# Kernel optimization log

Hardware: AMD Instinct MI355X
Metric: run time of the kernel (lower is better)

The kernel has to match this reference:

```python
import jax, jax.numpy as jnp
import numpy as np

B, E, H, V, KV = 64, 256, 512, 50257, 2048


def setup_inputs() -> dict:
    key = jax.random.key(0)
    ks = jax.random.split(key, 16)
    s_e = 1.0 / np.sqrt(E)
    s_h = 1.0 / np.sqrt(H)
    s_eh = 1.0 / np.sqrt(E + H)
    return {
        "input": jax.random.randint(ks[0], (B,), 0, V),
        "h0": jax.random.normal(ks[1], (B, H), jnp.float32),
        "c0": jax.random.normal(ks[2], (B, H), jnp.float32),
        "k": jax.random.normal(ks[3], (KV, E), jnp.float32),
        "context_vector": jax.random.normal(ks[4], (B, H), jnp.float32),
        # embedding table
        "embedding": jax.random.normal(ks[5], (V, E), jnp.float32) * 0.02,
        # LSTMCell params (PyTorch layout: gates ordered i,f,g,o)
        "W_ih": jax.random.uniform(ks[6], (4 * H, E), jnp.float32, -s_h, s_h),
        "b_ih": jax.random.uniform(ks[7], (4 * H,), jnp.float32, -s_h, s_h),
        "W_hh": jax.random.uniform(ks[8], (4 * H, H), jnp.float32, -s_h, s_h),
        "b_hh": jax.random.uniform(ks[9], (4 * H,), jnp.float32, -s_h, s_h),
        # attn_key MLP: Linear(E+H,E) -> tanh -> Linear(E,E) -> tanh -> Linear(E,1)
        "W1": jax.random.uniform(ks[10], (E, E + H), jnp.float32, -s_eh, s_eh),
        "b1": jnp.zeros((E,), jnp.float32),
        "W2": jax.random.uniform(ks[11], (E, E), jnp.float32, -s_e, s_e),
        "b2": jnp.zeros((E,), jnp.float32),
        "W3": jax.random.uniform(ks[12], (1, E), jnp.float32, -s_e, s_e),
        "b3": jnp.zeros((1,), jnp.float32),
        # output projection Linear(H, V)
        "W_out": jax.random.uniform(ks[13], (V, H), jnp.float32, -s_h, s_h),
        "b_out": jax.random.uniform(ks[14], (V,), jnp.float32, -s_h, s_h),
    }


def reference(input, h0, c0, k, context_vector, embedding, W_ih, b_ih, W_hh, b_hh,
              W1, b1, W2, b2, W3, b3, W_out, b_out):
    # embedding lookup (dropout in eval mode = identity)
    x = embedding[input]  # (B, E)
    # LSTMCell
    gates = x @ W_ih.T + b_ih + h0 @ W_hh.T + b_hh  # (B, 4H)
    i, f, g, o = jnp.split(gates, 4, axis=-1)
    i = jax.nn.sigmoid(i)
    f = jax.nn.sigmoid(f)
    g = jnp.tanh(g)
    o = jax.nn.sigmoid(o)
    c_t = f * c0 + i * g
    h_t = o * jnp.tanh(c_t)  # (B, H)
    # key attention: broadcast h_t over kv keys, keys over batch (torch.cat-repeat in original)
    h_b = jnp.broadcast_to(h_t[:, None, :], (B, KV, H))
    k_b = jnp.broadcast_to(k[None, :, :], (B, KV, E))
    feat = jnp.concatenate([h_b, k_b], axis=-1)  # (B, KV, H+E)
    u = jnp.tanh(feat @ W1.T + b1)
    u = jnp.tanh(u @ W2.T + b2)
    scores = (u @ W3.T + b3)[..., 0]  # (B, KV)
    # vocab logits; original pads V-KV zeros in front then adds -> scores hit last KV slots
    o_t = h_t @ W_out.T + b_out  # (B, V)
    o_t = o_t.at[:, V - KV:].add(scores)
    y_t = jax.nn.log_softmax(o_t, axis=-1)
    return (y_t, h_t, c_t)
```

## Files before the change

### kernel.cpp

```cpp
#include <hip/hip_runtime.h>
#include <math.h>

namespace {

constexpr int B = 64, E = 256, H = 512, V = 50257, KV = 2048;
constexpr int NOUT = (V + 63) / 64;
constexpr int PSTRIDE = 800;

typedef __bf16 bf16x8 __attribute__((ext_vector_type(8)));
typedef float f32x4 __attribute__((ext_vector_type(4)));

__device__ __forceinline__ float fast_tanh(float x) {
  float e = __expf(2.f * x);
  return 1.f - 2.f / (e + 1.f);
}
__device__ __forceinline__ float sigmoidf(float x) {
  return 1.f / (1.f + __expf(-x));
}
__device__ __forceinline__ f32x4 mfma16(bf16x8 a, bf16x8 b, f32x4 c) {
  return __builtin_amdgcn_mfma_f32_16x16x32_bf16(a, b, c, 0, 0, 0);
}

__global__ __launch_bounds__(256) void k_gates(const int* __restrict__ inp,
    const float* __restrict__ h0, const float* __restrict__ emb,
    const float* __restrict__ W_ih, const float* __restrict__ b_ih,
    const float* __restrict__ W_hh, const float* __restrict__ b_hh,
    float* __restrict__ gates) {
  int b = threadIdx.x & 63;
  int j = blockIdx.x * 4 + (threadIdx.x >> 6);
  j = __builtin_amdgcn_readfirstlane(j);
  int row = inp[b];
  const float* xr = emb + (long)row * E;
  const float* wi = W_ih + (long)j * E;
  const float* hr = h0 + b * H;
  const float* wh = W_hh + (long)j * H;
  float acc = b_ih[j] + b_hh[j];
#pragma unroll 8
  for (int t = 0; t < E / 4; ++t) {
    float4 x4 = ((const float4*)xr)[t];
    float4 w4 = ((const float4*)wi)[t];
    acc += x4.x * w4.x + x4.y * w4.y + x4.z * w4.z + x4.w * w4.w;
  }
#pragma unroll 8
  for (int t = 0; t < H / 4; ++t) {
    float4 h4 = ((const float4*)hr)[t];
    float4 w4 = ((const float4*)wh)[t];
    acc += h4.x * w4.x + h4.y * w4.y + h4.z * w4.z + h4.w * w4.w;
  }
  gates[j * B + b] = acc;
}

__global__ __launch_bounds__(256) void k_lstm(const float* __restrict__ gates,
    const float* __restrict__ c0, float* __restrict__ out_h, float* __restrict__ out_c,
    __bf16* __restrict__ hp) {
  int i = blockIdx.x * 256 + threadIdx.x;
  int b = i >> 9, hh = i & 511;
  float gi = gates[(hh)*B + b];
  float gf = gates[(hh + 512) * B + b];
  float gg = gates[(hh + 1024) * B + b];
  float go = gates[(hh + 1536) * B + b];
  float c = sigmoidf(gf) * c0[i] + sigmoidf(gi) * fast_tanh(gg);
  float h = sigmoidf(go) * fast_tanh(c);
  out_h[i] = h;
  out_c[i] = c;
  hp[((hh >> 3) * 64 + b) * 8 + (hh & 7)] = (__bf16)h;
}

__global__ __launch_bounds__(256) void k_prep(const float* __restrict__ h_t,
    const float* __restrict__ W1, const float* __restrict__ b1,
    const float* __restrict__ k, const float* __restrict__ W2,
    float* __restrict__ Ah, float* __restrict__ Kp, __bf16* __restrict__ W2p) {
  __shared__ float ks_[64][257];
  int bid = blockIdx.x;
  int t = threadIdx.x;
  if (bid < 64) {
    int b = t & 63;
    int e = bid * 4 + (t >> 6);
    e = __builtin_amdgcn_readfirstlane(e);
    const float* hr = h_t + b * H;
    const float* wr = W1 + (long)e * (E + H);
    float acc = b1[e];
#pragma unroll 8
    for (int q = 0; q < H / 4; ++q) {
      float4 h4 = ((const float4*)hr)[q];
      float4 w4 = ((const float4*)wr)[q];
      acc += h4.x * w4.x + h4.y * w4.y + h4.z * w4.z + h4.w * w4.w;
    }
    Ah[b * E + e] = acc;
  } else if (bid < 192) {
    int t2 = bid - 64;
    int kv0 = (t2 & 31) * 64;
    int e0 = (t2 >> 5) * 64;
    for (int i = 0; i < 16; ++i) {
      int idx = i * 256 + t;
      int rr = idx >> 6, cc = (idx & 63) * 4;
      float4 v = *(const float4*)(k + (kv0 + rr) * E + cc);
      ks_[rr][cc] = v.x; ks_[rr][cc + 1] = v.y; ks_[rr][cc + 2] = v.z; ks_[rr][cc + 3] = v.w;
    }
    __syncthreads();
    int r0 = (t >> 4);
    int c0 = (t & 15) * 4;
    float acc[4][4] = {};
    const float* w0 = W1 + (long)(e0 + c0) * (E + H) + H;
    for (int kk = 0; kk < 256; kk += 4) {
      float4 w[4];
#pragma unroll
      for (int c = 0; c < 4; ++c) w[c] = *(const float4*)(w0 + (long)c * (E + H) + kk);
#pragma unroll
      for (int q = 0; q < 4; ++q) {
#pragma unroll
        for (int r = 0; r < 4; ++r) {
          float kvv = ks_[r0 + 16 * r][kk + q];
#pragma unroll
          for (int c = 0; c < 4; ++c) acc[r][c] += kvv * ((const float*)&w[c])[q];
        }
      }
    }
    for (int r = 0; r < 4; ++r)
      for (int c = 0; c < 4; ++c)
        Kp[(kv0 + r0 + 16 * r) * E + e0 + c0 + c] = acc[r][c];
  } else {
    int idx = (bid - 192) * 256 + t;
    int kk = idx >> 8, n = idx & 255;
    W2p[((kk >> 3) * 256 + n) * 8 + (kk & 7)] = (__bf16)W2[n * 256 + kk];
  }
}

__global__ __launch_bounds__(256) void k_attn(const float* __restrict__ Ah,
    const float* __restrict__ Kp, const __bf16* __restrict__ W2p,
    const float* __restrict__ b2, const float* __restrict__ W3, const float* __restrict__ b3,
    float* __restrict__ scoresT) {
  __shared__ __align__(16) unsigned char lds_[64 * 256 * 2];
  int tid = threadIdx.x;
  int blk = blockIdx.x;
  int b = blk >> 5;
  int kv0 = (blk & 31) * 64;
  for (int i = 0; i < 8; ++i) {
    int idx = i * 256 + tid;
    int row = idx >> 5;
    int k0 = (idx & 31) * 8;
    const float* ap = Ah + b * E + k0;
    const float* kp = Kp + (kv0 + row) * E + k0;
    float4 a0 = *(const float4*)ap;
    float4 a1 = *(const float4*)(ap + 4);
    float4 p0 = *(const float4*)kp;
    float4 p1 = *(const float4*)(kp + 4);
    bf16x8 u;
    u[0] = (__bf16)fast_tanh(a0.x + p0.x);
    u[1] = (__bf16)fast_tanh(a0.y + p0.y);
    u[2] = (__bf16)fast_tanh(a0.z + p0.z);
    u[3] = (__bf16)fast_tanh(a0.w + p0.w);
    u[4] = (__bf16)fast_tanh(a1.x + p1.x);
    u[5] = (__bf16)fast_tanh(a1.y + p1.y);
    u[6] = (__bf16)fast_tanh(a1.z + p1.z);
    u[7] = (__bf16)fast_tanh(a1.w + p1.w);
    int byte = (row * 512 + k0 * 2) ^ ((row & 7) << 4);
    *(bf16x8*)(lds_ + byte) = u;
  }
  __syncthreads();
  int l = tid & 63, wc = tid >> 6;
  int lr = l & 15, lg = l >> 4;
  float b2v[4], w3v[4];
#pragma unroll
  for (int nf = 0; nf < 4; ++nf) {
    int col = wc * 64 + nf * 16 + lr;
    b2v[nf] = b2[col];
    w3v[nf] = W3[col];
  }
  f32x4 acc[4][4] = {};
  for (int ks = 0; ks < 8; ++ks) {
    bf16x8 a[4], bf[4];
#pragma unroll
    for (int mf = 0; mf < 4; ++mf) {
      int row = mf * 16 + lr;
      int byte = (row * 512 + (ks * 32 + lg * 8) * 2) ^ ((row & 7) << 4);
      a[mf] = *(const bf16x8*)(lds_ + byte);
    }
#pragma unroll
    for (int nf = 0; nf < 4; ++nf) {
      int col = wc * 64 + nf * 16 + lr;
      bf[nf] = *(const bf16x8*)(W2p + ((ks * 4 + lg) * 256 + col) * 8);
    }
#pragma unroll
    for (int mf = 0; mf < 4; ++mf)
#pragma unroll
      for (int nf = 0; nf < 4; ++nf)
        acc[mf][nf] = mfma16(a[mf], bf[nf], acc[mf][nf]);
  }
  float p[4][4];
#pragma unroll
  for (int mf = 0; mf < 4; ++mf)
#pragma unroll
    for (int r = 0; r < 4; ++r) p[mf][r] = 0.f;
#pragma unroll
  for (int mf = 0; mf < 4; ++mf)
#pragma unroll
    for (int nf = 0; nf < 4; ++nf)
#pragma unroll
      for (int r = 0; r < 4; ++r) {
        float u2 = fast_tanh(acc[mf][nf][r] + b2v[nf]);
        p[mf][r] += u2 * w3v[nf];
      }
#pragma unroll
  for (int off = 1; off < 16; off <<= 1)
#pragma unroll
    for (int mf = 0; mf < 4; ++mf)
#pragma unroll
      for (int r = 0; r < 4; ++r) p[mf][r] += __shfl_xor(p[mf][r], off);
  __syncthreads();
  float* red = (float*)lds_;
  if (lr == 0) {
#pragma unroll
    for (int mf = 0; mf < 4; ++mf)
#pragma unroll
      for (int r = 0; r < 4; ++r) red[(mf * 16 + lg * 4 + r) * 4 + wc] = p[mf][r];
  }
  __syncthreads();
  if (tid < 64) {
    float s = red[tid * 4 + 0] + red[tid * 4 + 1] + red[tid * 4 + 2] + red[tid * 4 + 3] + b3[0];
    scoresT[(kv0 + tid) * 64 + b] = s;
  }
}

__global__ __launch_bounds__(256) void k_out(const __bf16* __restrict__ hp,
    const float* __restrict__ W_out, const float* __restrict__ b_out,
    const float* __restrict__ scoresT, float* __restrict__ o,
    float* __restrict__ pm, float* __restrict__ ps) {
  __shared__ __align__(16) unsigned char lds_[64 * 256 * 2];
  __shared__ float rm[64][4], rs[64][4];
  int tid = threadIdx.x;
  int l = tid & 63, wn = tid >> 6;
  int lr = l & 15, lg = l >> 4;
  int col0 = blockIdx.x * 64;
  f32x4 acc[4] = {};
#pragma unroll
  for (int hh = 0; hh < 2; ++hh) {
    if (hh) __syncthreads();
#pragma unroll
    for (int i = 0; i < 8; ++i) {
      int u = i * 256 + tid;
      int row = u >> 5;
      int c16 = u & 31;
      int rr = col0 + row; if (rr > V - 1) rr = V - 1;
      const float* p = W_out + (long)rr * H + hh * 256 + c16 * 8;
      float4 w0 = *(const float4*)p;
      float4 w1 = *(const float4*)(p + 4);
      bf16x8 v;
      v[0] = (__bf16)w0.x; v[1] = (__bf16)w0.y; v[2] = (__bf16)w0.z; v[3] = (__bf16)w0.w;
      v[4] = (__bf16)w1.x; v[5] = (__bf16)w1.y; v[6] = (__bf16)w1.z; v[7] = (__bf16)w1.w;
      int byte = (row * 512 + c16 * 16) ^ ((row & 7) << 4);
      *(bf16x8*)(lds_ + byte) = v;
    }
    __syncthreads();
    int r = wn * 16 + lr;
    int rbase = r * 512;
    int rsw = (r & 7) << 4;
#pragma unroll
    for (int ks2 = 0; ks2 < 8; ++ks2) {
      int ksg = hh * 8 + ks2;
      bf16x8 a[4];
#pragma unroll
      for (int mf = 0; mf < 4; ++mf)
        a[mf] = *(const bf16x8*)(hp + ((ksg * 4 + lg) * 64 + mf * 16 + lr) * 8);
      bf16x8 bv = *(const bf16x8*)(lds_ + ((rbase + ks2 * 64 + lg * 16) ^ rsw));
#pragma unroll
      for (int mf = 0; mf < 4; ++mf) acc[mf] = mfma16(a[mf], bv, acc[mf]);
    }
  }
  __syncthreads();
  float (*vbuf)[65] = (float(*)[65])lds_;
  int col = col0 + wn * 16 + lr;
  bool valid = col < V;
  float bo = valid ? b_out[col] : 0.f;
  bool has = valid && col >= (V - KV);
  int scix = col - (V - KV);
#pragma unroll
  for (int mf = 0; mf < 4; ++mf)
#pragma unroll
    for (int r = 0; r < 4; ++r) {
      int m = mf * 16 + lg * 4 + r;
      float v = acc[mf][r] + bo;
      if (has) v += scoresT[scix * 64 + m];
      if (!valid) v = -1e30f;
      vbuf[m][wn * 16 + lr] = v;
    }
  __syncthreads();
  int nvalid = V - col0; if (nvalid > 64) nvalid = 64;
#pragma unroll
  for (int i = 0; i < 16; ++i) {
    int idx = i * 256 + tid;
    int m = idx >> 6, c = idx & 63;
    if (c < nvalid) o[(long)m * V + col0 + c] = vbuf[m][c];
  }
  int row = tid & 63, g = tid >> 6;
  float mm = -1e30f;
#pragma unroll
  for (int c = 0; c < 16; ++c) mm = fmaxf(mm, vbuf[row][g * 16 + c]);
  float ssum = 0.f;
#pragma unroll
  for (int c = 0; c < 16; ++c) ssum += __expf(vbuf[row][g * 16 + c] - mm);
  rm[row][g] = mm; rs[row][g] = ssum;
  __syncthreads();
  if (tid < 64) {
    float M = fmaxf(fmaxf(rm[tid][0], rm[tid][1]), fmaxf(rm[tid][2], rm[tid][3]));
    float S = 0.f;
#pragma unroll
    for (int g2 = 0; g2 < 4; ++g2) S += rs[tid][g2] * __expf(rm[tid][g2] - M);
    pm[tid * PSTRIDE + blockIdx.x] = M;
    ps[tid * PSTRIDE + blockIdx.x] = S;
  }
}

__global__ __launch_bounds__(256) void k_z(const float* __restrict__ pm,
    const float* __restrict__ ps, float* __restrict__ logZ) {
  int r = blockIdx.x;
  int tid = threadIdx.x;
  float m = -1e30f, s = 0.f;
  for (int p = tid; p < NOUT; p += 256) {
    float om = pm[r * PSTRIDE + p];
    float os = ps[r * PSTRIDE + p];
    float M = fmaxf(m, om);
    s = s * __expf(m - M) + os * __expf(om - M);
    m = M;
  }
#pragma unroll
  for (int off = 1; off < 64; off <<= 1) {
    float om = __shfl_xor(m, off);
    float os = __shfl_xor(s, off);
    float M = fmaxf(m, om);
    s = s * __expf(m - M) + os * __expf(om - M);
    m = M;
  }
  __shared__ float sm[4], ss[4];
  int w = tid >> 6;
  if ((tid & 63) == 0) { sm[w] = m; ss[w] = s; }
  __syncthreads();
  if (tid == 0) {
    m = sm[0]; s = ss[0];
    for (int i = 1; i < 4; ++i) {
      float M = fmaxf(m, sm[i]);
      s = s * __expf(m - M) + ss[i] * __expf(sm[i] - M);
      m = M;
    }
    logZ[r] = m + __logf(s);
  }
}

__global__ __launch_bounds__(256) void k_sub(float* __restrict__ o, const float* __restrict__ logZ) {
  int r = blockIdx.y;
  float z = logZ[r];
  int i0 = (blockIdx.x * 256 + threadIdx.x) * 4;
  float* row = o + (long)r * V;
  if (i0 + 3 < V) {
    float4 v = *(float4*)(row + i0);
    v.x -= z; v.y -= z; v.z -= z; v.w -= z;
    *(float4*)(row + i0) = v;
  } else {
    for (int i = i0; i < V; ++i) row[i] -= z;
  }
}

}

extern "C" void kernel_launch(void* const* d_in, const int* in_sizes, int n_in,
                              void* d_out, int out_size, void* d_ws, size_t ws_size,
                              hipStream_t stream) {
  const int* inp = (const int*)d_in[0];
  const float* h0 = (const float*)d_in[1];
  const float* c0 = (const float*)d_in[2];
  const float* kk = (const float*)d_in[3];
  const float* emb = (const float*)d_in[5];
  const float* W_ih = (const float*)d_in[6];
  const float* b_ih = (const float*)d_in[7];
  const float* W_hh = (const float*)d_in[8];
  const float* b_hh = (const float*)d_in[9];
  const float* W1 = (const float*)d_in[10];
  const float* b1 = (const float*)d_in[11];
  const float* W2 = (const float*)d_in[12];
  const float* b2 = (const float*)d_in[13];
  const float* W3 = (const float*)d_in[14];
  const float* b3 = (const float*)d_in[15];
  const float* W_out = (const float*)d_in[16];
  const float* b_out = (const float*)d_in[17];

  float* y = (float*)d_out;
  float* h_t = y + (size_t)B * V;
  float* c_t = h_t + (size_t)B * H;

  char* ws = (char*)d_ws;
  float* gates = (float*)ws;                 ws += (size_t)4 * H * B * 4;
  float* Ah = (float*)ws;                    ws += (size_t)B * E * 4;
  float* Kp = (float*)ws;                    ws += (size_t)KV * E * 4;
  float* scoresT = (float*)ws;               ws += (size_t)B * KV * 4;
  float* logZ = (float*)ws;                  ws += 256;
  float* pm = (float*)ws;                    ws += (size_t)B * PSTRIDE * 4;
  float* ps = (float*)ws;                    ws += (size_t)B * PSTRIDE * 4;
  __bf16* W2p = (__bf16*)ws;                 ws += (size_t)E * E * 2;
  __bf16* hp = (__bf16*)ws;                  ws += (size_t)B * H * 2;

  hipLaunchKernelGGL(k_gates, dim3(4 * H / 4), dim3(256), 0, stream,
                     inp, h0, emb, W_ih, b_ih, W_hh, b_hh, gates);
  hipLaunchKernelGGL(k_lstm, dim3(B * H / 256), dim3(256), 0, stream, gates, c0, h_t, c_t, hp);
  hipLaunchKernelGGL(k_prep, dim3(448), dim3(256), 0, stream,
                     h_t, W1, b1, kk, W2, Ah, Kp, W2p);
  hipLaunchKernelGGL(k_attn, dim3(B * KV / 64), dim3(256), 0, stream,
                     Ah, Kp, W2p, b2, W3, b3, scoresT);
  hipLaunchKernelGGL(k_out, dim3(NOUT), dim3(256), 0, stream,
                     hp, W_out, b_out, scoresT, y, pm, ps);
  hipLaunchKernelGGL(k_z, dim3(B), dim3(256), 0, stream, pm, ps, logZ);
  hipLaunchKernelGGL(k_sub, dim3((V + 1023) / 1024, B), dim3(256), 0, stream, y, logZ);
}
```

Before: 166.7 us.

## Split k_out K dimension across two wave groups with 512-thread blocks

```diff
diff --git a/kernel.cpp b/kernel.cpp
--- a/kernel.cpp
+++ b/kernel.cpp
@@ -222,90 +222,114 @@
   }
 }
 
-__global__ __launch_bounds__(256) void k_out(const __bf16* __restrict__ hp,
+__global__ __launch_bounds__(512) void k_out(const __bf16* __restrict__ hp,
     const float* __restrict__ W_out, const float* __restrict__ b_out,
     const float* __restrict__ scoresT, float* __restrict__ o,
     float* __restrict__ pm, float* __restrict__ ps) {
-  __shared__ __align__(16) unsigned char lds_[64 * 256 * 2];
-  __shared__ float rm[64][4], rs[64][4];
+  __shared__ __align__(16) unsigned char lds_[64 * 512 * 2];
+  __shared__ float rm[64][8], rs[64][8];
   int tid = threadIdx.x;
-  int l = tid & 63, wn = tid >> 6;
-  int lr = l & 15, lg = l >> 4;
+  int wave = tid >> 6;
+  int kh = wave >> 2;
+  int wn = wave & 3;
+  int l = tid & 63;
+  int lr = l & 15, lg = (l >> 4) & 3;
   int col0 = blockIdx.x * 64;
+#pragma unroll
+  for (int i = 0; i < 8; ++i) {
+    int u = i * 512 + tid;
+    int row = u >> 6;
+    int c16 = u & 63;
+    int rr = col0 + row; if (rr > V - 1) rr = V - 1;
+    const float* p = W_out + (long)rr * H + c16 * 8;
+    float4 w0 = *(const float4*)p;
+    float4 w1 = *(const float4*)(p + 4);
+    bf16x8 v;
+    v[0] = (__bf16)w0.x; v[1] = (__bf16)w0.y; v[2] = (__bf16)w0.z; v[3] = (__bf16)w0.w;
+    v[4] = (__bf16)w1.x; v[5] = (__bf16)w1.y; v[6] = (__bf16)w1.z; v[7] = (__bf16)w1.w;
+    int byte = (row * 1024 + c16 * 16) ^ ((row & 7) << 4);
+    *(bf16x8*)(lds_ + byte) = v;
+  }
+  __syncthreads();
+  int r = wn * 16 + lr;
+  int rbase = r * 1024;
+  int rsw = (r & 7) << 4;
   f32x4 acc[4] = {};
-#pragma unroll
-  for (int hh = 0; hh < 2; ++hh) {
-    if (hh) __syncthreads();
-#pragma unroll
-    for (int i = 0; i < 8; ++i) {
-      int u = i * 256 + tid;
-      int row = u >> 5;
-      int c16 = u & 31;
-      int rr = col0 + row; if (rr > V - 1) rr = V - 1;
-      const float* p = W_out + (long)rr * H + hh * 256 + c16 * 8;
-      float4 w0 = *(const float4*)p;
-      float4 w1 = *(const float4*)(p + 4);
-      bf16x8 v;
-      v[0] = (__bf16)w0.x; v[1] = (__bf16)w0.y; v[2] = (__bf16)w0.z; v[3] = (__bf16)w0.w;
-      v[4] = (__bf16)w1.x; v[5] = (__bf16)w1.y; v[6] = (__bf16)w1.z; v[7] = (__bf16)w1.w;
-      int byte = (row * 512 + c16 * 16) ^ ((row & 7) << 4);
-      *(bf16x8*)(lds_ + byte) = v;
-    }
-    __syncthreads();
-    int r = wn * 16 + lr;
-    int rbase = r * 512;
-    int rsw = (r & 7) << 4;
-#pragma unroll
-    for (int ks2 = 0; ks2 < 8; ++ks2) {
-      int ksg = hh * 8 + ks2;
-      bf16x8 a[4];
+  bf16x8 a_n[4], b_n;
+  {
+    int ksg = kh * 8;
+#pragma unroll
+    for (int mf = 0; mf < 4; ++mf)
+      a_n[mf] = *(const bf16x8*)(hp + ((ksg * 4 + lg) * 64 + mf * 16 + lr) * 8);
+    b_n = *(const bf16x8*)(lds_ + ((rbase + ksg * 64 + lg * 16) ^ rsw));
+  }
+#pragma unroll
+  for (int ks2 = 0; ks2 < 8; ++ks2) {
+    bf16x8 a_c[4]; bf16x8 b_c = b_n;
+#pragma unroll
+    for (int mf = 0; mf < 4; ++mf) a_c[mf] = a_n[mf];
+    if (ks2 < 7) {
+      int ksg = kh * 8 + ks2 + 1;
 #pragma unroll
       for (int mf = 0; mf < 4; ++mf)
-        a[mf] = *(const bf16x8*)(hp + ((ksg * 4 + lg) * 64 + mf * 16 + lr) * 8);
-      bf16x8 bv = *(const bf16x8*)(lds_ + ((rbase + ks2 * 64 + lg * 16) ^ rsw));
-#pragma unroll
-      for (int mf = 0; mf < 4; ++mf) acc[mf] = mfma16(a[mf], bv, acc[mf]);
-    }
-  }
-  __syncthreads();
-  float (*vbuf)[65] = (float(*)[65])lds_;
-  int col = col0 + wn * 16 + lr;
-  bool valid = col < V;
-  float bo = valid ? b_out[col] : 0.f;
-  bool has = valid && col >= (V - KV);
-  int scix = col - (V - KV);
-#pragma unroll
-  for (int mf = 0; mf < 4; ++mf)
-#pragma unroll
-    for (int r = 0; r < 4; ++r) {
-      int m = mf * 16 + lg * 4 + r;
-      float v = acc[mf][r] + bo;
-      if (has) v += scoresT[scix * 64 + m];
-      if (!valid) v = -1e30f;
-      vbuf[m][wn * 16 + lr] = v;
-    }
+        a_n[mf] = *(const bf16x8*)(hp + ((ksg * 4 + lg) * 64 + mf * 16 + lr) * 8);
+      b_n = *(const bf16x8*)(lds_ + ((rbase + ksg * 64 + lg * 16) ^ rsw));
+    }
+#pragma unroll
+    for (int mf = 0; mf < 4; ++mf) acc[mf] = mfma16(a_c[mf], b_c, acc[mf]);
+  }
+  __syncthreads();
+  float* red = (float*)lds_;
+  if (kh == 1) {
+#pragma unroll
+    for (int mf = 0; mf < 4; ++mf)
+#pragma unroll
+      for (int rr2 = 0; rr2 < 4; ++rr2)
+        red[(mf * 16 + lg * 4 + rr2) * 64 + wn * 16 + lr] = acc[mf][rr2];
+  }
+  __syncthreads();
+  float (*vbuf)[65] = (float(*)[65])(lds_ + 16384);
+  if (kh == 0) {
+    int col = col0 + wn * 16 + lr;
+    bool valid = col < V;
+    float bo = valid ? b_out[col] : 0.f;
+    bool has = valid && col >= (V - KV);
+    int scix = col - (V - KV);
+#pragma unroll
+    for (int mf = 0; mf < 4; ++mf)
+#pragma unroll
+      for (int rr2 = 0; rr2 < 4; ++rr2) {
+        int m = mf * 16 + lg * 4 + rr2;
+        float v = acc[mf][rr2] + red[m * 64 + wn * 16 + lr] + bo;
+        if (has) v += scoresT[scix * 64 + m];
+        if (!valid) v = -1e30f;
+        vbuf[m][wn * 16 + lr] = v;
+      }
+  }
   __syncthreads();
   int nvalid = V - col0; if (nvalid > 64) nvalid = 64;
 #pragma unroll
-  for (int i = 0; i < 16; ++i) {
-    int idx = i * 256 + tid;
+  for (int i = 0; i < 8; ++i) {
+    int idx = i * 512 + tid;
     int m = idx >> 6, c = idx & 63;
     if (c < nvalid) o[(long)m * V + col0 + c] = vbuf[m][c];
   }
   int row = tid & 63, g = tid >> 6;
   float mm = -1e30f;
 #pragma unroll
-  for (int c = 0; c < 16; ++c) mm = fmaxf(mm, vbuf[row][g * 16 + c]);
+  for (int c = 0; c < 8; ++c) mm = fmaxf(mm, vbuf[row][g * 8 + c]);
   float ssum = 0.f;
 #pragma unroll
-  for (int c = 0; c < 16; ++c) ssum += __expf(vbuf[row][g * 16 + c] - mm);
+  for (int c = 0; c < 8; ++c) ssum += __expf(vbuf[row][g * 8 + c] - mm);
   rm[row][g] = mm; rs[row][g] = ssum;
   __syncthreads();
   if (tid < 64) {
-    float M = fmaxf(fmaxf(rm[tid][0], rm[tid][1]), fmaxf(rm[tid][2], rm[tid][3]));
+    float M = rm[tid][0];
+#pragma unroll
+    for (int g2 = 1; g2 < 8; ++g2) M = fmaxf(M, rm[tid][g2]);
     float S = 0.f;
 #pragma unroll
-    for (int g2 = 0; g2 < 4; ++g2) S += rs[tid][g2] * __expf(rm[tid][g2] - M);
+    for (int g2 = 0; g2 < 8; ++g2) S += rs[tid][g2] * __expf(rm[tid][g2] - M);
     pm[tid * PSTRIDE + blockIdx.x] = M;
     ps[tid * PSTRIDE + blockIdx.x] = S;
   }
@@ -405,7 +429,7 @@
                      h_t, W1, b1, kk, W2, Ah, Kp, W2p);
   hipLaunchKernelGGL(k_attn, dim3(B * KV / 64), dim3(256), 0, stream,
                      Ah, Kp, W2p, b2, W3, b3, scoresT);
-  hipLaunchKernelGGL(k_out, dim3(NOUT), dim3(256), 0, stream,
+  hipLaunchKernelGGL(k_out, dim3(NOUT), dim3(512), 0, stream,
                      hp, W_out, b_out, scoresT, y, pm, ps);
   hipLaunchKernelGGL(k_z, dim3(B), dim3(256), 0, stream, pm, ps, logZ);
   hipLaunchKernelGGL(k_sub, dim3((V + 1023) / 1024, B), dim3(256), 0, stream, y, logZ);
```

After: 170.2 us. 2.1% more time.

## Pre-pack W_out into bf16 k-major layout in a separate kernel

Applied to the files above, without the earlier changes.

```diff
diff --git a/kernel.cpp b/kernel.cpp
--- a/kernel.cpp
+++ b/kernel.cpp
@@ -5,6 +5,7 @@
 
 constexpr int B = 64, E = 256, H = 512, V = 50257, KV = 2048;
 constexpr int NOUT = (V + 63) / 64;
+constexpr int VP = NOUT * 64;
 constexpr int PSTRIDE = 800;
 
 typedef __bf16 bf16x8 __attribute__((ext_vector_type(8)));
@@ -19,6 +20,36 @@
 }
 __device__ __forceinline__ f32x4 mfma16(bf16x8 a, bf16x8 b, f32x4 c) {
   return __builtin_amdgcn_mfma_f32_16x16x32_bf16(a, b, c, 0, 0, 0);
+}
+
+__global__ __launch_bounds__(256) void k_packw(const float* __restrict__ W_out,
+                                               __bf16* __restrict__ Wp) {
+  __shared__ __align__(16) unsigned char lds_[64 * 512 * 2];
+  int tid = threadIdx.x;
+  int col0 = blockIdx.x * 64;
+#pragma unroll
+  for (int i = 0; i < 16; ++i) {
+    int u = i * 256 + tid;
+    int row = u >> 6, k8 = u & 63;
+    int rr = col0 + row; if (rr > V - 1) rr = V - 1;
+    const float* p = W_out + (long)rr * H + k8 * 8;
+    float4 w0 = *(const float4*)p;
+    float4 w1 = *(const float4*)(p + 4);
+    bf16x8 v;
+    v[0] = (__bf16)w0.x; v[1] = (__bf16)w0.y; v[2] = (__bf16)w0.z; v[3] = (__bf16)w0.w;
+    v[4] = (__bf16)w1.x; v[5] = (__bf16)w1.y; v[6] = (__bf16)w1.z; v[7] = (__bf16)w1.w;
+    int byte = (row * 1024 + k8 * 16) ^ ((row & 7) << 4);
+    *(bf16x8*)(lds_ + byte) = v;
+  }
+  __syncthreads();
+#pragma unroll
+  for (int i = 0; i < 16; ++i) {
+    int u = i * 256 + tid;
+    int k8 = u >> 6, colt = u & 63;
+    int byte = (colt * 1024 + k8 * 16) ^ ((colt & 7) << 4);
+    bf16x8 v = *(const bf16x8*)(lds_ + byte);
+    *(bf16x8*)(Wp + ((long)k8 * VP + col0 + colt) * 8) = v;
+  }
 }
 
 __global__ __launch_bounds__(256) void k_gates(const int* __restrict__ inp,
@@ -223,53 +254,27 @@
 }
 
 __global__ __launch_bounds__(256) void k_out(const __bf16* __restrict__ hp,
-    const float* __restrict__ W_out, const float* __restrict__ b_out,
+    const __bf16* __restrict__ Wp, const float* __restrict__ b_out,
     const float* __restrict__ scoresT, float* __restrict__ o,
     float* __restrict__ pm, float* __restrict__ ps) {
-  __shared__ __align__(16) unsigned char lds_[64 * 256 * 2];
+  __shared__ float vbuf[64][65];
   __shared__ float rm[64][4], rs[64][4];
   int tid = threadIdx.x;
   int l = tid & 63, wn = tid >> 6;
   int lr = l & 15, lg = l >> 4;
   int col0 = blockIdx.x * 64;
+  int col = col0 + wn * 16 + lr;
   f32x4 acc[4] = {};
 #pragma unroll
-  for (int hh = 0; hh < 2; ++hh) {
-    if (hh) __syncthreads();
-#pragma unroll
-    for (int i = 0; i < 8; ++i) {
-      int u = i * 256 + tid;
-      int row = u >> 5;
-      int c16 = u & 31;
-      int rr = col0 + row; if (rr > V - 1) rr = V - 1;
-      const float* p = W_out + (long)rr * H + hh * 256 + c16 * 8;
-      float4 w0 = *(const float4*)p;
-      float4 w1 = *(const float4*)(p + 4);
-      bf16x8 v;
-      v[0] = (__bf16)w0.x; v[1] = (__bf16)w0.y; v[2] = (__bf16)w0.z; v[3] = (__bf16)w0.w;
-      v[4] = (__bf16)w1.x; v[5] = (__bf16)w1.y; v[6] = (__bf16)w1.z; v[7] = (__bf16)w1.w;
-      int byte = (row * 512 + c16 * 16) ^ ((row & 7) << 4);
-      *(bf16x8*)(lds_ + byte) = v;
-    }
-    __syncthreads();
-    int r = wn * 16 + lr;
-    int rbase = r * 512;
-    int rsw = (r & 7) << 4;
-#pragma unroll
-    for (int ks2 = 0; ks2 < 8; ++ks2) {
-      int ksg = hh * 8 + ks2;
-      bf16x8 a[4];
-#pragma unroll
-      for (int mf = 0; mf < 4; ++mf)
-        a[mf] = *(const bf16x8*)(hp + ((ksg * 4 + lg) * 64 + mf * 16 + lr) * 8);
-      bf16x8 bv = *(const bf16x8*)(lds_ + ((rbase + ks2 * 64 + lg * 16) ^ rsw));
-#pragma unroll
-      for (int mf = 0; mf < 4; ++mf) acc[mf] = mfma16(a[mf], bv, acc[mf]);
-    }
-  }
-  __syncthreads();
-  float (*vbuf)[65] = (float(*)[65])lds_;
-  int col = col0 + wn * 16 + lr;
+  for (int ks = 0; ks < 16; ++ks) {
+    bf16x8 a[4];
+#pragma unroll
+    for (int mf = 0; mf < 4; ++mf)
+      a[mf] = *(const bf16x8*)(hp + ((ks * 4 + lg) * 64 + mf * 16 + lr) * 8);
+    bf16x8 bv = *(const bf16x8*)(Wp + ((long)(ks * 4 + lg) * VP + col) * 8);
+#pragma unroll
+    for (int mf = 0; mf < 4; ++mf) acc[mf] = mfma16(a[mf], bv, acc[mf]);
+  }
   bool valid = col < V;
   float bo = valid ? b_out[col] : 0.f;
   bool has = valid && col >= (V - KV);
@@ -397,7 +402,10 @@
   float* ps = (float*)ws;                    ws += (size_t)B * PSTRIDE * 4;
   __bf16* W2p = (__bf16*)ws;                 ws += (size_t)E * E * 2;
   __bf16* hp = (__bf16*)ws;                  ws += (size_t)B * H * 2;
-
+  ws = (char*)(((size_t)ws + 255) & ~(size_t)255);
+  __bf16* Wp = (__bf16*)ws;                  ws += (size_t)VP * H * 2;
+
+  hipLaunchKernelGGL(k_packw, dim3(NOUT), dim3(256), 0, stream, W_out, Wp);
   hipLaunchKernelGGL(k_gates, dim3(4 * H / 4), dim3(256), 0, stream,
                      inp, h0, emb, W_ih, b_ih, W_hh, b_hh, gates);
   hipLaunchKernelGGL(k_lstm, dim3(B * H / 256), dim3(256), 0, stream, gates, c0, h_t, c_t, hp);
@@ -406,7 +414,7 @@
   hipLaunchKernelGGL(k_attn, dim3(B * KV / 64), dim3(256), 0, stream,
                      Ah, Kp, W2p, b2, W3, b3, scoresT);
   hipLaunchKernelGGL(k_out, dim3(NOUT), dim3(256), 0, stream,
-                     hp, W_out, b_out, scoresT, y, pm, ps);
+                     hp, Wp, b_out, scoresT, y, pm, ps);
   hipLaunchKernelGGL(k_z, dim3(B), dim3(256), 0, stream, pm, ps, logZ);
   hipLaunchKernelGGL(k_sub, dim3((V + 1023) / 1024, B), dim3(256), 0, stream, y, logZ);
 }
```

Result: slower. 182.9 us (+9.7%).

## Merge all stages into one cooperative persistent kernel with grid syncs

Applied to the files above, without the earlier changes.

```diff
diff --git a/kernel.cpp b/kernel.cpp
--- a/kernel.cpp
+++ b/kernel.cpp
@@ -1,5 +1,8 @@
 #include <hip/hip_runtime.h>
+#include <hip/hip_cooperative_groups.h>
 #include <math.h>
+
+namespace cg = cooperative_groups;
 
 namespace {
 
@@ -21,63 +24,109 @@
   return __builtin_amdgcn_mfma_f32_16x16x32_bf16(a, b, c, 0, 0, 0);
 }
 
-__global__ __launch_bounds__(256) void k_gates(const int* __restrict__ inp,
-    const float* __restrict__ h0, const float* __restrict__ emb,
+__global__ __launch_bounds__(256, 3) void mono(
+    const int* __restrict__ inp, const float* __restrict__ h0,
+    const float* __restrict__ c0, const float* __restrict__ kkey,
+    const float* __restrict__ emb,
     const float* __restrict__ W_ih, const float* __restrict__ b_ih,
     const float* __restrict__ W_hh, const float* __restrict__ b_hh,
-    float* __restrict__ gates) {
-  int b = threadIdx.x & 63;
-  int j = blockIdx.x * 4 + (threadIdx.x >> 6);
-  j = __builtin_amdgcn_readfirstlane(j);
-  int row = inp[b];
-  const float* xr = emb + (long)row * E;
-  const float* wi = W_ih + (long)j * E;
-  const float* hr = h0 + b * H;
-  const float* wh = W_hh + (long)j * H;
-  float acc = b_ih[j] + b_hh[j];
+    const float* __restrict__ W1, const float* __restrict__ b1,
+    const float* __restrict__ W2, const float* __restrict__ b2,
+    const float* __restrict__ W3, const float* __restrict__ b3,
+    const float* __restrict__ W_out, const float* __restrict__ b_out,
+    float* __restrict__ y, float* __restrict__ h_t, float* __restrict__ c_t,
+    float* __restrict__ Ah, float* __restrict__ Kp, float* __restrict__ scoresT,
+    float* __restrict__ logZ, float* __restrict__ pm, float* __restrict__ ps,
+    __bf16* __restrict__ W2p, __bf16* __restrict__ hp) {
+  __shared__ __align__(16) unsigned char SM[32896];
+  __shared__ float g4[4][64];
+  __shared__ float rm[64][4], rs[64][4];
+  __shared__ float sm2[4], ss2[4];
+  cg::grid_group grid = cg::this_grid();
+  int tid = threadIdx.x, bid = blockIdx.x, nb = gridDim.x;
+
+  for (int t = bid; t < 1024; t += nb) {
+    if (t < 512) {
+      int hh = t;
+      int jq = tid >> 6, b = tid & 63;
+      int j = jq * 512 + hh;
+      int row = inp[b];
+      const float* xr = emb + (long)row * E;
+      const float* wi = W_ih + (long)j * E;
+      const float* hr = h0 + (long)b * H;
+      const float* wh = W_hh + (long)j * H;
+      float acc = b_ih[j] + b_hh[j];
 #pragma unroll 8
-  for (int t = 0; t < E / 4; ++t) {
-    float4 x4 = ((const float4*)xr)[t];
-    float4 w4 = ((const float4*)wi)[t];
-    acc += x4.x * w4.x + x4.y * w4.y + x4.z * w4.z + x4.w * w4.w;
-  }
+      for (int q = 0; q < E / 4; ++q) {
+        float4 x4 = ((const float4*)xr)[q];
+        float4 w4 = ((const float4*)wi)[q];
+        acc += x4.x * w4.x + x4.y * w4.y + x4.z * w4.z + x4.w * w4.w;
+      }
 #pragma unroll 8
-  for (int t = 0; t < H / 4; ++t) {
-    float4 h4 = ((const float4*)hr)[t];
-    float4 w4 = ((const float4*)wh)[t];
-    acc += h4.x * w4.x + h4.y * w4.y + h4.z * w4.z + h4.w * w4.w;
-  }
-  gates[j * B + b] = acc;
-}
-
-__global__ __launch_bounds__(256) void k_lstm(const float* __restrict__ gates,
-    const float* __restrict__ c0, float* __restrict__ out_h, float* __restrict__ out_c,
-    __bf16* __restrict__ hp) {
-  int i = blockIdx.x * 256 + threadIdx.x;
-  int b = i >> 9, hh = i & 511;
-  float gi = gates[(hh)*B + b];
-  float gf = gates[(hh + 512) * B + b];
-  float gg = gates[(hh + 1024) * B + b];
-  float go = gates[(hh + 1536) * B + b];
-  float c = sigmoidf(gf) * c0[i] + sigmoidf(gi) * fast_tanh(gg);
-  float h = sigmoidf(go) * fast_tanh(c);
-  out_h[i] = h;
-  out_c[i] = c;
-  hp[((hh >> 3) * 64 + b) * 8 + (hh & 7)] = (__bf16)h;
-}
-
-__global__ __launch_bounds__(256) void k_prep(const float* __restrict__ h_t,
-    const float* __restrict__ W1, const float* __restrict__ b1,
-    const float* __restrict__ k, const float* __restrict__ W2,
-    float* __restrict__ Ah, float* __restrict__ Kp, __bf16* __restrict__ W2p) {
-  __shared__ float ks_[64][257];
-  int bid = blockIdx.x;
-  int t = threadIdx.x;
+      for (int q = 0; q < H / 4; ++q) {
+        float4 h4 = ((const float4*)hr)[q];
+        float4 w4 = ((const float4*)wh)[q];
+        acc += h4.x * w4.x + h4.y * w4.y + h4.z * w4.z + h4.w * w4.w;
+      }
+      g4[jq][b] = acc;
+      __syncthreads();
+      if (tid < 64) {
+        int bb = tid;
+        float cc = sigmoidf(g4[1][bb]) * c0[bb * H + hh] +
+                   sigmoidf(g4[0][bb]) * fast_tanh(g4[2][bb]);
+        float hv = sigmoidf(g4[3][bb]) * fast_tanh(cc);
+        h_t[bb * H + hh] = hv;
+        c_t[bb * H + hh] = cc;
+        hp[((hh >> 3) * 64 + bb) * 8 + (hh & 7)] = (__bf16)hv;
+      }
+    } else if (t < 768) {
+      float(*ks2)[257] = (float(*)[257])SM;
+      int kt = t - 512;
+      int kv0 = (kt & 63) * 32;
+      int e0 = (kt >> 6) * 64;
+#pragma unroll
+      for (int i = 0; i < 8; ++i) {
+        int idx = i * 256 + tid;
+        int rr = idx >> 6, ccc = (idx & 63) * 4;
+        float4 v = *(const float4*)(kkey + (long)(kv0 + rr) * E + ccc);
+        ks2[rr][ccc] = v.x; ks2[rr][ccc + 1] = v.y;
+        ks2[rr][ccc + 2] = v.z; ks2[rr][ccc + 3] = v.w;
+      }
+      __syncthreads();
+      int r0 = tid >> 4;
+      int c0e = (tid & 15) * 4;
+      float acc[2][4] = {};
+      const float* w0 = W1 + (long)(e0 + c0e) * (E + H) + H;
+      for (int kk = 0; kk < 256; kk += 4) {
+        float4 w[4];
+#pragma unroll
+        for (int c = 0; c < 4; ++c) w[c] = *(const float4*)(w0 + (long)c * (E + H) + kk);
+#pragma unroll
+        for (int q = 0; q < 4; ++q) {
+#pragma unroll
+          for (int r = 0; r < 2; ++r) {
+            float kvv = ks2[r0 + 16 * r][kk + q];
+#pragma unroll
+            for (int c = 0; c < 4; ++c) acc[r][c] += kvv * ((const float*)&w[c])[q];
+          }
+        }
+      }
+      for (int r = 0; r < 2; ++r)
+        for (int c = 0; c < 4; ++c)
+          Kp[(long)(kv0 + r0 + 16 * r) * E + e0 + c0e + c] = acc[r][c];
+    } else {
+      int idx = (t - 768) * 256 + tid;
+      int kk = idx >> 8, n = idx & 255;
+      W2p[((kk >> 3) * 256 + n) * 8 + (kk & 7)] = (__bf16)W2[n * 256 + kk];
+    }
+    __syncthreads();
+  }
+  grid.sync();
+
   if (bid < 64) {
-    int b = t & 63;
-    int e = bid * 4 + (t >> 6);
-    e = __builtin_amdgcn_readfirstlane(e);
-    const float* hr = h_t + b * H;
+    int b = tid & 63;
+    int e = bid * 4 + (tid >> 6);
+    const float* hr = h_t + (long)b * H;
     const float* wr = W1 + (long)e * (E + H);
     float acc = b1[e];
 #pragma unroll 8
@@ -87,276 +136,234 @@
       acc += h4.x * w4.x + h4.y * w4.y + h4.z * w4.z + h4.w * w4.w;
     }
     Ah[b * E + e] = acc;
-  } else if (bid < 192) {
-    int t2 = bid - 64;
-    int kv0 = (t2 & 31) * 64;
-    int e0 = (t2 >> 5) * 64;
-    for (int i = 0; i < 16; ++i) {
-      int idx = i * 256 + t;
-      int rr = idx >> 6, cc = (idx & 63) * 4;
-      float4 v = *(const float4*)(k + (kv0 + rr) * E + cc);
-      ks_[rr][cc] = v.x; ks_[rr][cc + 1] = v.y; ks_[rr][cc + 2] = v.z; ks_[rr][cc + 3] = v.w;
-    }
-    __syncthreads();
-    int r0 = (t >> 4);
-    int c0 = (t & 15) * 4;
-    float acc[4][4] = {};
-    const float* w0 = W1 + (long)(e0 + c0) * (E + H) + H;
-    for (int kk = 0; kk < 256; kk += 4) {
-      float4 w[4];
-#pragma unroll
-      for (int c = 0; c < 4; ++c) w[c] = *(const float4*)(w0 + (long)c * (E + H) + kk);
-#pragma unroll
-      for (int q = 0; q < 4; ++q) {
-#pragma unroll
-        for (int r = 0; r < 4; ++r) {
-          float kvv = ks_[r0 + 16 * r][kk + q];
-#pragma unroll
-          for (int c = 0; c < 4; ++c) acc[r][c] += kvv * ((const float*)&w[c])[q];
-        }
-      }
-    }
-    for (int r = 0; r < 4; ++r)
-      for (int c = 0; c < 4; ++c)
-        Kp[(kv0 + r0 + 16 * r) * E + e0 + c0 + c] = acc[r][c];
-  } else {
-    int idx = (bid - 192) * 256 + t;
-    int kk = idx >> 8, n = idx & 255;
-    W2p[((kk >> 3) * 256 + n) * 8 + (kk & 7)] = (__bf16)W2[n * 256 + kk];
-  }
-}
-
-__global__ __launch_bounds__(256) void k_attn(const float* __restrict__ Ah,
-    const float* __restrict__ Kp, const __bf16* __restrict__ W2p,
-    const float* __restrict__ b2, const float* __restrict__ W3, const float* __restrict__ b3,
-    float* __restrict__ scoresT) {
-  __shared__ __align__(16) unsigned char lds_[64 * 256 * 2];
-  int tid = threadIdx.x;
-  int blk = blockIdx.x;
-  int b = blk >> 5;
-  int kv0 = (blk & 31) * 64;
-  for (int i = 0; i < 8; ++i) {
-    int idx = i * 256 + tid;
-    int row = idx >> 5;
-    int k0 = (idx & 31) * 8;
-    const float* ap = Ah + b * E + k0;
-    const float* kp = Kp + (kv0 + row) * E + k0;
-    float4 a0 = *(const float4*)ap;
-    float4 a1 = *(const float4*)(ap + 4);
-    float4 p0 = *(const float4*)kp;
-    float4 p1 = *(const float4*)(kp + 4);
-    bf16x8 u;
-    u[0] = (__bf16)fast_tanh(a0.x + p0.x);
-    u[1] = (__bf16)fast_tanh(a0.y + p0.y);
-    u[2] = (__bf16)fast_tanh(a0.z + p0.z);
-    u[3] = (__bf16)fast_tanh(a0.w + p0.w);
-    u[4] = (__bf16)fast_tanh(a1.x + p1.x);
-    u[5] = (__bf16)fast_tanh(a1.y + p1.y);
-    u[6] = (__bf16)fast_tanh(a1.z + p1.z);
-    u[7] = (__bf16)fast_tanh(a1.w + p1.w);
-    int byte = (row * 512 + k0 * 2) ^ ((row & 7) << 4);
-    *(bf16x8*)(lds_ + byte) = u;
-  }
-  __syncthreads();
-  int l = tid & 63, wc = tid >> 6;
-  int lr = l & 15, lg = l >> 4;
-  float b2v[4], w3v[4];
-#pragma unroll
-  for (int nf = 0; nf < 4; ++nf) {
-    int col = wc * 64 + nf * 16 + lr;
-    b2v[nf] = b2[col];
-    w3v[nf] = W3[col];
-  }
-  f32x4 acc[4][4] = {};
-  for (int ks = 0; ks < 8; ++ks) {
-    bf16x8 a[4], bf[4];
-#pragma unroll
-    for (int mf = 0; mf < 4; ++mf) {
-      int row = mf * 16 + lr;
-      int byte = (row * 512 + (ks * 32 + lg * 8) * 2) ^ ((row & 7) << 4);
-      a[mf] = *(const bf16x8*)(lds_ + byte);
-    }
+  }
+  grid.sync();
+
+  for (int t = bid; t < 2048; t += nb) {
+    int b = t >> 5;
+    int kv0 = (t & 31) * 64;
+    for (int i = 0; i < 8; ++i) {
+      int idx = i * 256 + tid;
+      int row = idx >> 5;
+      int k0 = (idx & 31) * 8;
+      const float* ap = Ah + b * E + k0;
+      const float* kp = Kp + (long)(kv0 + row) * E + k0;
+      float4 a0 = *(const float4*)ap;
+      float4 a1 = *(const float4*)(ap + 4);
+      float4 p0 = *(const float4*)kp;
+      float4 p1 = *(const float4*)(kp + 4);
+      bf16x8 u;
+      u[0] = (__bf16)fast_tanh(a0.x + p0.x);
+      u[1] = (__bf16)fast_tanh(a0.y + p0.y);
+      u[2] = (__bf16)fast_tanh(a0.z + p0.z);
+      u[3] = (__bf16)fast_tanh(a0.w + p0.w);
+      u[4] = (__bf16)fast_tanh(a1.x + p1.x);
+      u[5] = (__bf16)fast_tanh(a1.y + p1.y);
+      u[6] = (__bf16)fast_tanh(a1.z + p1.z);
+      u[7] = (__bf16)fast_tanh(a1.w + p1.w);
+      int byte = (row * 512 + k0 * 2) ^ ((row & 7) << 4);
+      *(bf16x8*)(SM + byte) = u;
+    }
+    __syncthreads();
+    int l = tid & 63, wc = tid >> 6;
+    int lr = l & 15, lg = l >> 4;
+    float b2v[4], w3v[4];
 #pragma unroll
     for (int nf = 0; nf < 4; ++nf) {
       int col = wc * 64 + nf * 16 + lr;
-      bf[nf] = *(const bf16x8*)(W2p + ((ks * 4 + lg) * 256 + col) * 8);
-    }
+      b2v[nf] = b2[col];
+      w3v[nf] = W3[col];
+    }
+    f32x4 acc[4][4] = {};
+    for (int ks = 0; ks < 8; ++ks) {
+      bf16x8 a[4], bf[4];
+#pragma unroll
+      for (int mf = 0; mf < 4; ++mf) {
+        int row = mf * 16 + lr;
+        int byte = (row * 512 + (ks * 32 + lg * 8) * 2) ^ ((row & 7) << 4);
+        a[mf] = *(const bf16x8*)(SM + byte);
+      }
+#pragma unroll
+      for (int nf = 0; nf < 4; ++nf) {
+        int col = wc * 64 + nf * 16 + lr;
+        bf[nf] = *(const bf16x8*)(W2p + ((ks * 4 + lg) * 256 + col) * 8);
+      }
+#pragma unroll
+      for (int mf = 0; mf < 4; ++mf)
+#pragma unroll
+        for (int nf = 0; nf < 4; ++nf)
+          acc[mf][nf] = mfma16(a[mf], bf[nf], acc[mf][nf]);
+    }
+    float p[4][4];
 #pragma unroll
     for (int mf = 0; mf < 4; ++mf)
 #pragma unroll
+      for (int r = 0; r < 4; ++r) p[mf][r] = 0.f;
+#pragma unroll
+    for (int mf = 0; mf < 4; ++mf)
+#pragma unroll
       for (int nf = 0; nf < 4; ++nf)
-        acc[mf][nf] = mfma16(a[mf], bf[nf], acc[mf][nf]);
-  }
-  float p[4][4];
-#pragma unroll
-  for (int mf = 0; mf < 4; ++mf)
-#pragma unroll
-    for (int r = 0; r < 4; ++r) p[mf][r] = 0.f;
-#pragma unroll
-  for (int mf = 0; mf < 4; ++mf)
-#pragma unroll
-    for (int nf = 0; nf < 4; ++nf)
+#pragma unroll
+        for (int r = 0; r < 4; ++r) {
+          float u2 = fast_tanh(acc[mf][nf][r] + b2v[nf]);
+          p[mf][r] += u2 * w3v[nf];
+        }
+#pragma unroll
+    for (int off = 1; off < 16; off <<= 1)
+#pragma unroll
+      for (int mf = 0; mf < 4; ++mf)
+#pragma unroll
+        for (int r = 0; r < 4; ++r) p[mf][r] += __shfl_xor(p[mf][r], off);
+    __syncthreads();
+    float* red = (float*)SM;
+    if (lr == 0) {
+#pragma unroll
+      for (int mf = 0; mf < 4; ++mf)
+#pragma unroll
+        for (int r = 0; r < 4; ++r) red[(mf * 16 + lg * 4 + r) * 4 + wc] = p[mf][r];
+    }
+    __syncthreads();
+    if (tid < 64) {
+      float s = red[tid * 4 + 0] + red[tid * 4 + 1] + red[tid * 4 + 2] + red[tid * 4 + 3] + b3[0];
+      scoresT[(long)(kv0 + tid) * 64 + b] = s;
+    }
+    __syncthreads();
+  }
+  grid.sync();
+
+  for (int t = bid; t < NOUT; t += nb) {
+    int l = tid & 63, wn = tid >> 6;
+    int lr = l & 15, lg = l >> 4;
+    int col0 = t * 64;
+    f32x4 acc[4] = {};
+#pragma unroll
+    for (int hhf = 0; hhf < 2; ++hhf) {
+      if (hhf) __syncthreads();
+#pragma unroll
+      for (int i = 0; i < 8; ++i) {
+        int u = i * 256 + tid;
+        int row = u >> 5;
+        int c16 = u & 31;
+        int rr = col0 + row; if (rr > V - 1) rr = V - 1;
+        const float* p = W_out + (long)rr * H + hhf * 256 + c16 * 8;
+        float4 w0 = *(const float4*)p;
+        float4 w1 = *(const float4*)(p + 4);
+        bf16x8 v;
+        v[0] = (__bf16)w0.x; v[1] = (__bf16)w0.y; v[2] = (__bf16)w0.z; v[3] = (__bf16)w0.w;
+        v[4] = (__bf16)w1.x; v[5] = (__bf16)w1.y; v[6] = (__bf16)w1.z; v[7] = (__bf16)w1.w;
+        int byte = (row * 512 + c16 * 16) ^ ((row & 7) << 4);
+        *(bf16x8*)(SM + byte) = v;
+      }
+      __syncthreads();
+      int r = wn * 16 + lr;
+      int rbase = r * 512;
+      int rsw = (r & 7) << 4;
+#pragma unroll
+      for (int ks2 = 0; ks2 < 8; ++ks2) {
+        int ksg = hhf * 8 + ks2;
+        bf16x8 a[4];
+#pragma unroll
+        for (int mf = 0; mf < 4; ++mf)
+          a[mf] = *(const bf16x8*)(hp + ((ksg * 4 + lg) * 64 + mf * 16 + lr) * 8);
+        bf16x8 bv = *(const bf16x8*)(SM + ((rbase + ks2 * 64 + lg * 16) ^ rsw));
+#pragma unroll
+        for (int mf = 0; mf < 4; ++mf) acc[mf] = mfma16(a[mf], bv, acc[mf]);
+      }
+    }
+    __syncthreads();
+    float(*vbuf)[65] = (float(*)[65])SM;
+    int col = col0 + wn * 16 + lr;
+    bool valid = col < V;
+    float bo = valid ? b_out[col] : 0.f;
+    bool has = valid && col >= (V - KV);
+    int scix = col - (V - KV);
+#pragma unroll
+    for (int mf = 0; mf < 4; ++mf)
 #pragma unroll
       for (int r = 0; r < 4; ++r) {
-        float u2 = fast_tanh(acc[mf][nf][r] + b2v[nf]);
-        p[mf][r] += u2 * w3v[nf];
-      }
-#pragma unroll
-  for (int off = 1; off < 16; off <<= 1)
-#pragma unroll
-    for (int mf = 0; mf < 4; ++mf)
-#pragma unroll
-      for (int r = 0; r < 4; ++r) p[mf][r] += __shfl_xor(p[mf][r], off);
-  __syncthreads();
-  float* red = (float*)lds_;
-  if (lr == 0) {
-#pragma unroll
-    for (int mf = 0; mf < 4; ++mf)
-#pragma unroll
-      for (int r = 0; r < 4; ++r) red[(mf * 16 + lg * 4 + r) * 4 + wc] = p[mf][r];
-  }
-  __syncthreads();
-  if (tid < 64) {
-    float s = red[tid * 4 + 0] + red[tid * 4 + 1] + red[tid * 4 + 2] + red[tid * 4 + 3] + b3[0];
-    scoresT[(kv0 + tid) * 64 + b] = s;
-  }
-}
-
-__global__ __launch_bounds__(256) void k_out(const __bf16* __restrict__ hp,
-    const float* __restrict__ W_out, const float* __restrict__ b_out,
-    const float* __restrict__ scoresT, float* __restrict__ o,
-    float* __restrict__ pm, float* __restrict__ ps) {
-  __shared__ __align__(16) unsigned char lds_[64 * 256 * 2];
-  __shared__ float rm[64][4], rs[64][4];
-  int tid = threadIdx.x;
-  int l = tid & 63, wn = tid >> 6;
-  int lr = l & 15, lg = l >> 4;
-  int col0 = blockIdx.x * 64;
-  f32x4 acc[4] = {};
-#pragma unroll
-  for (int hh = 0; hh < 2; ++hh) {
-    if (hh) __syncthreads();
-#pragma unroll
-    for (int i = 0; i < 8; ++i) {
-      int u = i * 256 + tid;
-      int row = u >> 5;
-      int c16 = u & 31;
-      int rr = col0 + row; if (rr > V - 1) rr = V - 1;
-      const float* p = W_out + (long)rr * H + hh * 256 + c16 * 8;
-      float4 w0 = *(const float4*)p;
-      float4 w1 = *(const float4*)(p + 4);
-      bf16x8 v;
-      v[0] = (__bf16)w0.x; v[1] = (__bf16)w0.y; v[2] = (__bf16)w0.z; v[3] = (__bf16)w0.w;
-      v[4] = (__bf16)w1.x; v[5] = (__bf16)w1.y; v[6] = (__bf16)w1.z; v[7] = (__bf16)w1.w;
-      int byte = (row * 512 + c16 * 16) ^ ((row & 7) << 4);
-      *(bf16x8*)(lds_ + byte) = v;
-    }
-    __syncthreads();
-    int r = wn * 16 + lr;
-    int rbase = r * 512;
-    int rsw = (r & 7) << 4;
-#pragma unroll
-    for (int ks2 = 0; ks2 < 8; ++ks2) {
-      int ksg = hh * 8 + ks2;
-      bf16x8 a[4];
-#pragma unroll
-      for (int mf = 0; mf < 4; ++mf)
-        a[mf] = *(const bf16x8*)(hp + ((ksg * 4 + lg) * 64 + mf * 16 + lr) * 8);
-      bf16x8 bv = *(const bf16x8*)(lds_ + ((rbase + ks2 * 64 + lg * 16) ^ rsw));
-#pragma unroll
-      for (int mf = 0; mf < 4; ++mf) acc[mf] = mfma16(a[mf], bv, acc[mf]);
-    }
-  }
-  __syncthreads();
-  float (*vbuf)[65] = (float(*)[65])lds_;
-  int col = col0 + wn * 16 + lr;
-  bool valid = col < V;
-  float bo = valid ? b_out[col] : 0.f;
-  bool has = valid && col >= (V - KV);
-  int scix = col - (V - KV);
-#pragma unroll
-  for (int mf = 0; mf < 4; ++mf)
-#pragma unroll
-    for (int r = 0; r < 4; ++r) {
-      int m = mf * 16 + lg * 4 + r;
-      float v = acc[mf][r] + bo;
-      if (has) v += scoresT[scix * 64 + m];
-      if (!valid) v = -1e30f;
-      vbuf[m][wn * 16 + lr] = v;
-    }
-  __syncthreads();
-  int nvalid = V - col0; if (nvalid > 64) nvalid = 64;
-#pragma unroll
-  for (int i = 0; i < 16; ++i) {
-    int idx = i * 256 + tid;
-    int m = idx >> 6, c = idx & 63;
-    if (c < nvalid) o[(long)m * V + col0 + c] = vbuf[m][c];
-  }
-  int row = tid & 63, g = tid >> 6;
-  float mm = -1e30f;
-#pragma unroll
-  for (int c = 0; c < 16; ++c) mm = fmaxf(mm, vbuf[row][g * 16 + c]);
-  float ssum = 0.f;
-#pragma unroll
-  for (int c = 0; c < 16; ++c) ssum += __expf(vbuf[row][g * 16 + c] - mm);
-  rm[row][g] = mm; rs[row][g] = ssum;
-  __syncthreads();
-  if (tid < 64) {
-    float M = fmaxf(fmaxf(rm[tid][0], rm[tid][1]), fmaxf(rm[tid][2], rm[tid][3]));
-    float S = 0.f;
-#pragma unroll
-    for (int g2 = 0; g2 < 4; ++g2) S += rs[tid][g2] * __expf(rm[tid][g2] - M);
-    pm[tid * PSTRIDE + blockIdx.x] = M;
-    ps[tid * PSTRIDE + blockIdx.x] = S;
-  }
-}
-
-__global__ __launch_bounds__(256) void k_z(const float* __restrict__ pm,
-    const float* __restrict__ ps, float* __restrict__ logZ) {
-  int r = blockIdx.x;
-  int tid = threadIdx.x;
-  float m = -1e30f, s = 0.f;
-  for (int p = tid; p < NOUT; p += 256) {
-    float om = pm[r * PSTRIDE + p];
-    float os = ps[r * PSTRIDE + p];
-    float M = fmaxf(m, om);
-    s = s * __expf(m - M) + os * __expf(om - M);
-    m = M;
-  }
-#pragma unroll
-  for (int off = 1; off < 64; off <<= 1) {
-    float om = __shfl_xor(m, off);
-    float os = __shfl_xor(s, off);
-    float M = fmaxf(m, om);
-    s = s * __expf(m - M) + os * __expf(om - M);
-    m = M;
-  }
-  __shared__ float sm[4], ss[4];
-  int w = tid >> 6;
-  if ((tid & 63) == 0) { sm[w] = m; ss[w] = s; }
-  __syncthreads();
-  if (tid == 0) {
-    m = sm[0]; s = ss[0];
-    for (int i = 1; i < 4; ++i) {
-      float M = fmaxf(m, sm[i]);
-      s = s * __expf(m - M) + ss[i] * __expf(sm[i] - M);
+        int m = mf * 16 + lg * 4 + r;
+        float v = acc[mf][r] + bo;
+        if (has) v += scoresT[(long)scix * 64 + m];
+        if (!valid) v = -1e30f;
+        vbuf[m][wn * 16 + lr] = v;
+      }
+    __syncthreads();
+    int nvalid = V - col0; if (nvalid > 64) nvalid = 64;
+#pragma unroll
+    for (int i = 0; i < 16; ++i) {
+      int idx = i * 256 + tid;
+      int m = idx >> 6, c = idx & 63;
+      if (c < nvalid) y[(long)m * V + col0 + c] = vbuf[m][c];
+    }
+    int row = tid & 63, g = tid >> 6;
+    float mm = -1e30f;
+#pragma unroll
+    for (int c = 0; c < 16; ++c) mm = fmaxf(mm, vbuf[row][g * 16 + c]);
+    float ssum = 0.f;
+#pragma unroll
+    for (int c = 0; c < 16; ++c) ssum += __expf(vbuf[row][g * 16 + c] - mm);
+    rm[row][g] = mm; rs[row][g] = ssum;
+    __syncthreads();
+    if (tid < 64) {
+      float M = fmaxf(fmaxf(rm[tid][0], rm[tid][1]), fmaxf(rm[tid][2], rm[tid][3]));
+      float S = 0.f;
+#pragma unroll
+      for (int g2 = 0; g2 < 4; ++g2) S += rs[tid][g2] * __expf(rm[tid][g2] - M);
+      pm[tid * PSTRIDE + t] = M;
+      ps[tid * PSTRIDE + t] = S;
+    }
+    __syncthreads();
+  }
+  grid.sync();
+
+  if (bid < 64) {
+    int r = bid;
+    float m = -1e30f, s = 0.f;
+    for (int p = tid; p < NOUT; p += 256) {
+      float om = pm[r * PSTRIDE + p];
+      float os = ps[r * PSTRIDE + p];
+      float M = fmaxf(m, om);
+      s = s * __expf(m - M) + os * __expf(om - M);
       m = M;
     }
-    logZ[r] = m + __logf(s);
-  }
-}
-
-__global__ __launch_bounds__(256) void k_sub(float* __restrict__ o, const float* __restrict__ logZ) {
-  int r = blockIdx.y;
-  float z = logZ[r];
-  int i0 = (blockIdx.x * 256 + threadIdx.x) * 4;
-  float* row = o + (long)r * V;
-  if (i0 + 3 < V) {
-    float4 v = *(float4*)(row + i0);
-    v.x -= z; v.y -= z; v.z -= z; v.w -= z;
-    *(float4*)(row + i0) = v;
-  } else {
-    for (int i = i0; i < V; ++i) row[i] -= z;
+#pragma unroll
+    for (int off = 1; off < 64; off <<= 1) {
+      float om = __shfl_xor(m, off);
+      float os = __shfl_xor(s, off);
+      float M = fmaxf(m, om);
+      s = s * __expf(m - M) + os * __expf(om - M);
+      m = M;
+    }
+    int w = tid >> 6;
+    if ((tid & 63) == 0) { sm2[w] = m; ss2[w] = s; }
+    __syncthreads();
+    if (tid == 0) {
+      m = sm2[0]; s = ss2[0];
+      for (int i = 1; i < 4; ++i) {
+        float M = fmaxf(m, sm2[i]);
+        s = s * __expf(m - M) + ss2[i] * __expf(sm2[i] - M);
+        m = M;
+      }
+      logZ[r] = m + __logf(s);
+    }
+  }
+  grid.sync();
+
+  constexpr int SLOTS = (V + 3) / 4;
+  int total4 = 64 * SLOTS;
+  int stride = nb * 256;
+  for (int i4 = bid * 256 + tid; i4 < total4; i4 += stride) {
+    int r = i4 / SLOTS;
+    int c_el = (i4 - r * SLOTS) * 4;
+    float z = logZ[r];
+    float* rowp = y + (long)r * V;
+    if (c_el + 3 < V) {
+      float4 v = *(float4*)(rowp + c_el);
+      v.x -= z; v.y -= z; v.z -= z; v.w -= z;
+      *(float4*)(rowp + c_el) = v;
+    } else {
+      for (int c2 = c_el; c2 < V; ++c2) rowp[c2] -= z;
+    }
   }
 }
 
@@ -368,7 +375,7 @@
   const int* inp = (const int*)d_in[0];
   const float* h0 = (const float*)d_in[1];
   const float* c0 = (const float*)d_in[2];
-  const float* kk = (const float*)d_in[3];
+  const float* kkey = (const float*)d_in[3];
   const float* emb = (const float*)d_in[5];
   const float* W_ih = (const float*)d_in[6];
   const float* b_ih = (const float*)d_in[7];
@@ -388,7 +395,6 @@
   float* c_t = h_t + (size_t)B * H;
 
   char* ws = (char*)d_ws;
-  float* gates = (float*)ws;                 ws += (size_t)4 * H * B * 4;
   float* Ah = (float*)ws;                    ws += (size_t)B * E * 4;
   float* Kp = (float*)ws;                    ws += (size_t)KV * E * 4;
   float* scoresT = (float*)ws;               ws += (size_t)B * KV * 4;
@@ -398,15 +404,21 @@
   __bf16* W2p = (__bf16*)ws;                 ws += (size_t)E * E * 2;
   __bf16* hp = (__bf16*)ws;                  ws += (size_t)B * H * 2;
 
-  hipLaunchKernelGGL(k_gates, dim3(4 * H / 4), dim3(256), 0, stream,
-                     inp, h0, emb, W_ih, b_ih, W_hh, b_hh, gates);
-  hipLaunchKernelGGL(k_lstm, dim3(B * H / 256), dim3(256), 0, stream, gates, c0, h_t, c_t, hp);
-  hipLaunchKernelGGL(k_prep, dim3(448), dim3(256), 0, stream,
-                     h_t, W1, b1, kk, W2, Ah, Kp, W2p);
-  hipLaunchKernelGGL(k_attn, dim3(B * KV / 64), dim3(256), 0, stream,
-                     Ah, Kp, W2p, b2, W3, b3, scoresT);
-  hipLaunchKernelGGL(k_out, dim3(NOUT), dim3(256), 0, stream,
-                     hp, W_out, b_out, scoresT, y, pm, ps);
-  hipLaunchKernelGGL(k_z, dim3(B), dim3(256), 0, stream, pm, ps, logZ);
-  hipLaunchKernelGGL(k_sub, dim3((V + 1023) / 1024, B), dim3(256), 0, stream, y, logZ);
-}
+  int occ = 0;
+  if (hipOccupancyMaxActiveBlocksPerMultiprocessor(&occ, (const void*)mono, 256, 0)
+          != hipSuccess || occ < 1)
+    occ = 2;
+  int grid = occ * 256;
+  if (grid > 768) grid = 768;
+
+  void* args[] = {
+    (void*)&inp, (void*)&h0, (void*)&c0, (void*)&kkey, (void*)&emb,
+    (void*)&W_ih, (void*)&b_ih, (void*)&W_hh, (void*)&b_hh,
+    (void*)&W1, (void*)&b1, (void*)&W2, (void*)&b2, (void*)&W3, (void*)&b3,
+    (void*)&W_out, (void*)&b_out,
+    (void*)&y, (void*)&h_t, (void*)&c_t,
+    (void*)&Ah, (void*)&Kp, (void*)&scoresT, (void*)&logZ,
+    (void*)&pm, (void*)&ps, (void*)&W2p, (void*)&hp
+  };
+  hipLaunchCooperativeKernel((const void*)mono, dim3(grid), dim3(256), args, 0, stream);
+}
```

Measured after the change: 479.8 us. 2.88x slower.
